# Performance work log

Measured on AMD Instinct MI355X. Metric: run time of the kernel, lower is better.

## Reference

```python
import jax, jax.numpy as jnp
import numpy as np

N = 50000      # total packed nodes
E = 1600000    # edges (no self loops; layers add them)
G = 64         # graphs in the batch
F_IN = 24      # raw node feature dim
D = 64         # hidden dim
H = 4          # attention heads
C = D // H     # 16 channels per head
L = 3          # GAT layers
NEG = 0.2      # LeakyReLU negative slope (GATv2 default)
EPS = 1e-5     # LayerNorm eps


def setup_inputs() -> dict:
    key = jax.random.key(0)
    ks = jax.random.split(key, 16)
    x = jax.random.normal(ks[0], (N, F_IN), jnp.float32)
    src = jax.random.randint(ks[1], (E,), 0, N)
    dst = jax.random.randint(ks[2], (E,), 0, N)
    dst = jnp.where(dst == src, (dst + 1) % N, dst)  # keep edge list self-loop free
    edge_index = jnp.stack([src, dst]).astype(jnp.int32)
    batch = jnp.sort(jax.random.randint(ks[3], (N,), 0, G)).astype(jnp.int32)
    s = 0.1
    return dict(
        x=x, edge_index=edge_index, batch=batch,
        w_in=jax.random.normal(ks[4], (F_IN, D), jnp.float32) * s,
        b_in=jnp.zeros((D,), jnp.float32),
        w_l=jax.random.normal(ks[5], (L, D, D), jnp.float32) * s,
        b_l=jnp.zeros((L, D), jnp.float32),
        w_r=jax.random.normal(ks[6], (L, D, D), jnp.float32) * s,
        b_r=jnp.zeros((L, D), jnp.float32),
        att=jax.random.normal(ks[7], (L, H, C), jnp.float32) * s,
        b_gat=jnp.zeros((L, D), jnp.float32),
        ln_g=jnp.ones((L, D), jnp.float32),
        ln_b=jnp.zeros((L, D), jnp.float32),
        w_g1=jax.random.normal(ks[8], (D, D // 2), jnp.float32) * s,
        b_g1=jnp.zeros((D // 2,), jnp.float32),
        w_g2=jax.random.normal(ks[9], (D // 2, 1), jnp.float32) * s,
        b_g2=jnp.zeros((1,), jnp.float32),
        w_out=jax.random.normal(ks[10], (D, D), jnp.float32) * s,
        b_out=jnp.zeros((D,), jnp.float32),
    )


def _layernorm(h, g, b):
    m = h.mean(-1, keepdims=True)
    v = ((h - m) ** 2).mean(-1, keepdims=True)
    return (h - m) * jax.lax.rsqrt(v + EPS) * g + b


def _gatv2(h, src, dst, wl, bl, wr, br, att, bg):
    n = h.shape[0]
    xl = (h @ wl + bl).reshape(n, H, C)   # source transform
    xr = (h @ wr + br).reshape(n, H, C)   # target transform
    # edge scores: att . leaky_relu(xl[j] + xr[i])  -> [E', H]
    e = jnp.sum(jax.nn.leaky_relu(xl[src] + xr[dst], NEG) * att, axis=-1)
    emax = jax.ops.segment_max(e, dst, num_segments=n)
    ex = jnp.exp(e - emax[dst])
    denom = jax.ops.segment_sum(ex, dst, num_segments=n)
    alpha = ex / denom[dst]               # segment softmax over incoming edges
    out = jax.ops.segment_sum(alpha[:, :, None] * xl[src], dst, num_segments=n)
    return out.reshape(n, D) + bg


def reference(x, edge_index, batch, w_in, b_in, w_l, b_l, w_r, b_r, att, b_gat,
              ln_g, ln_b, w_g1, b_g1, w_g2, b_g2, w_out, b_out):
    n = x.shape[0]
    loops = jnp.arange(n, dtype=edge_index.dtype)
    src = jnp.concatenate([edge_index[0], loops])  # add self loops once
    dst = jnp.concatenate([edge_index[1], loops])
    h = jax.nn.relu(x @ w_in + b_in)
    for i in range(L):
        res = h
        h = _gatv2(h, src, dst, w_l[i], b_l[i], w_r[i], b_r[i], att[i], b_gat[i])
        h = _layernorm(h + res, ln_g[i], ln_b[i])
        if i < L - 1:
            h = jax.nn.relu(h)
    # GlobalAttention pooling: gate MLP -> per-graph softmax -> weighted sum
    gate = jax.nn.relu(h @ w_g1 + b_g1) @ w_g2 + b_g2  # [N, 1]
    gmax = jax.ops.segment_max(gate, batch, num_segments=G)
    ge = jnp.exp(gate - gmax[batch])
    gs = jax.ops.segment_sum(ge, batch, num_segments=G)
    a = ge / jnp.where(gs > 0, gs, 1.0)[batch]
    emb = jax.ops.segment_sum(a * h, batch, num_segments=G)  # [G, D]
    return jax.nn.relu(emb @ w_out + b_out)
```

## Files before the change

kernel.cpp:

```cpp
#include <hip/hip_runtime.h>

#define NEGS   0.2f
#define LN_EPS 1e-5f
#define BSH    7
#define BN     128
#define TILE   4096
#define LOG2E  1.44269504f

typedef const float* __restrict__ fp;
typedef _Float16 v2h __attribute__((ext_vector_type(2)));
typedef _Float16 v8h __attribute__((ext_vector_type(8)));
typedef float    v4f __attribute__((ext_vector_type(4)));

__device__ __forceinline__ v2h u2h(unsigned u){ union{unsigned u; v2h h;} c; c.u = u; return c.h; }
__device__ __forceinline__ unsigned h2u(v2h h){ union{v2h h; unsigned u;} c; c.h = h; return c.u; }

template<int CTRL>
__device__ __forceinline__ float dppadd(float x){
  int y = __builtin_amdgcn_update_dpp(0, __float_as_int(x), CTRL, 0xF, 0xF, true);
  return x + __int_as_float(y);
}
__device__ __forceinline__ float hsum8(float s){
  s = dppadd<0xB1>(s);
  s = dppadd<0x4E>(s);
  s = dppadd<0x141>(s);
  return s;
}
__device__ __forceinline__ float edge_w(v2h v, v2h xrv, v2h att2, float negm8){
  v2h t = v + xrv;
  t = __builtin_elementwise_max(t, t * (_Float16)NEGS);
  float s = hsum8(__builtin_amdgcn_fdot2(t, att2, negm8, false));
  return __builtin_amdgcn_exp2f(s);
}

__global__ __launch_bounds__(256) void k_in(fp x, fp w, fp b, float* __restrict__ h,
                                            unsigned* __restrict__ h16, int N){
  __shared__ float ws[24*64];
  __shared__ float bs[64];
  __shared__ float xs[4][24];
  int tid = threadIdx.x;
  for (int i = tid; i < 24*64; i += 256) ws[i] = w[i];
  if (tid < 64) bs[tid] = b[tid];
  int r = tid >> 6, c = tid & 63;
  int row = blockIdx.x*4 + r;
  if (c < 24 && row < N) xs[r][c] = x[row*24 + c];
  __syncthreads();
  float acc = bs[c];
  #pragma unroll
  for (int k = 0; k < 24; ++k) acc = fmaf(xs[r][k], ws[k*64 + c], acc);
  float y = fmaxf(acc, 0.f);
  float y1 = __shfl_down(y, 1);
  if (row < N){
    h[(size_t)row*64 + c] = y;
    if (!(c & 1)){
      v2h p; p.x = (_Float16)y; p.y = (_Float16)y1;
      h16[(size_t)row*32 + (c >> 1)] = h2u(p);
    }
  }
}

__global__ __launch_bounds__(256) void k_wprep(fp w_l, fp w_r, _Float16* __restrict__ wf){
  int lm = blockIdx.x;
  const float* src = ((lm & 1) ? w_r : w_l) + (lm >> 1)*4096;
  _Float16* dst = wf + lm*4096;
  for (int d = threadIdx.x; d < 4096; d += 256){
    int j = d & 7, l = (d >> 3) & 63, kc = (d >> 9) & 1, nt = d >> 10;
    int k = kc*32 + (l >> 4)*8 + j;
    int n = nt*16 + (l & 15);
    dst[d] = (_Float16)src[k*64 + n];
  }
}

__global__ __launch_bounds__(256) void t_hist(const int* __restrict__ dstA, int* __restrict__ counts,
                                              int E, int K, int ntiles){
  __shared__ int hist[512];
  int t = blockIdx.x, tid = threadIdx.x;
  for (int i = tid; i < K; i += 256) hist[i] = 0;
  __syncthreads();
  int e0 = t*TILE, e1 = min(e0 + TILE, E);
  for (int e = e0 + tid; e < e1; e += 256)
    atomicAdd(&hist[dstA[e] >> BSH], 1);
  __syncthreads();
  for (int i = tid; i < K; i += 256) counts[i*ntiles + t] = hist[i];
}

__global__ __launch_bounds__(512) void s_scan_tiles(int* __restrict__ counts, int* __restrict__ btotal,
                                                    int ntiles){
  __shared__ int s[512];
  int b = blockIdx.x, tid = threadIdx.x;
  int v = (tid < ntiles) ? counts[b*ntiles + tid] : 0;
  s[tid] = v;
  __syncthreads();
  for (int off = 1; off < 512; off <<= 1){
    int t = (tid >= off) ? s[tid - off] : 0;
    __syncthreads();
    s[tid] += t;
    __syncthreads();
  }
  if (tid < ntiles) counts[b*ntiles + tid] = s[tid] - v;
  if (tid == 511) btotal[b] = s[511];
}

__global__ __launch_bounds__(512) void s_scan_buckets(const int* __restrict__ btotal,
                                                      int* __restrict__ bbase, int K, int E){
  __shared__ int s[512];
  int tid = threadIdx.x;
  int v = (tid < K) ? btotal[tid] : 0;
  s[tid] = v;
  __syncthreads();
  for (int off = 1; off < 512; off <<= 1){
    int t = (tid >= off) ? s[tid - off] : 0;
    __syncthreads();
    s[tid] += t;
    __syncthreads();
  }
  if (tid < K) bbase[tid] = s[tid] - v;
  if (tid == 0) bbase[K] = E;
}

__global__ __launch_bounds__(256) void t_scatter(const int* __restrict__ srcA, const int* __restrict__ dstA,
                                                 const int* __restrict__ counts, const int* __restrict__ bbase,
                                                 unsigned* __restrict__ packed, int E, int K, int ntiles){
  __shared__ int gb[512];
  __shared__ int cur[512];
  int t = blockIdx.x, tid = threadIdx.x;
  for (int i = tid; i < K; i += 256){
    gb[i] = bbase[i] + counts[i*ntiles + t];
    cur[i] = 0;
  }
  __syncthreads();
  int e0 = t*TILE, e1 = min(e0 + TILE, E);
  for (int e = e0 + tid; e < e1; e += 256){
    int d = dstA[e], sv = srcA[e];
    int b = d >> BSH;
    int p = atomicAdd(&cur[b], 1);
    packed[gb[b] + p] = ((unsigned)(d & (BN-1)) << 25) | (unsigned)sv;
  }
}

__global__ __launch_bounds__(256) void k_fine(const unsigned* __restrict__ packed, const int* __restrict__ bbase,
                                              int* __restrict__ row_ptr, int* __restrict__ col, int N, int K){
  __shared__ int hist[BN];
  __shared__ int excl[BN];
  int b = blockIdx.x, tid = threadIdx.x;
  int node0 = b << BSH;
  int e_base = bbase[b], e_end = bbase[b+1];
  if (tid < BN) hist[tid] = 0;
  __syncthreads();
  for (int e = e_base + tid; e < e_end; e += 256)
    atomicAdd(&hist[packed[e] >> 25], 1);
  __syncthreads();
  int v = (tid < BN) ? hist[tid] : 0;
  if (tid < BN) excl[tid] = v;
  __syncthreads();
  for (int off = 1; off < BN; off <<= 1){
    int t2 = 0;
    if (tid < BN && tid >= off) t2 = excl[tid - off];
    __syncthreads();
    if (tid < BN) excl[tid] += t2;
    __syncthreads();
  }
  int nn = min(BN, N - node0);
  if (tid < nn) row_ptr[node0 + tid] = e_base + excl[tid] - v;
  if (b == K-1 && tid == 0) row_ptr[N] = e_end;
  if (tid < BN) hist[tid] = excl[tid] - v;
  __syncthreads();
  for (int e = e_base + tid; e < e_end; e += 256){
    unsigned u = packed[e];
    int dl = u >> 25;
    int p = atomicAdd(&hist[dl], 1);
    col[e_base + p] = (int)(u & 0x1FFFFFFu);
  }
}

__global__ __launch_bounds__(256) void k_xfm(const unsigned* __restrict__ h16,
                                             const _Float16* __restrict__ wf,
                                             fp blg, fp brg,
                                             unsigned* __restrict__ xl16, unsigned* __restrict__ xr16, int N){
  int tid = threadIdx.x, wave = tid >> 6, lane = tid & 63;
  int quad = lane >> 4, ln = lane & 15;
  int m0 = blockIdx.x*64 + wave*16;
  if (m0 >= N) return;
  int m = m0 + ln;
  bool mv = m < N;
  v8h a0 = {}, a1 = {};
  if (mv){
    a0 = *(const v8h*)&h16[(size_t)m*32 + quad*4];
    a1 = *(const v8h*)&h16[(size_t)m*32 + 16 + quad*4];
  }
  #pragma unroll
  for (int mat = 0; mat < 2; ++mat){
    const _Float16* wb = wf + mat*4096;
    fp bias = mat ? brg : blg;
    unsigned* dst = mat ? xr16 : xl16;
    #pragma unroll
    for (int nt = 0; nt < 4; ++nt){
      v8h b0 = *(const v8h*)&wb[nt*1024 + lane*8];
      v8h b1 = *(const v8h*)&wb[nt*1024 + 512 + lane*8];
      float bv = bias[nt*16 + ln];
      v4f acc = {bv, bv, bv, bv};
      acc = __builtin_amdgcn_mfma_f32_16x16x32_f16(a0, b0, acc, 0, 0, 0);
      acc = __builtin_amdgcn_mfma_f32_16x16x32_f16(a1, b1, acc, 0, 0, 0);
      #pragma unroll
      for (int r = 0; r < 4; ++r){
        float partner = __shfl_xor(acc[r], 1);
        int node = m0 + quad*4 + r;
        if (!(lane & 1) && node < N){
          v2h p; p.x = (_Float16)acc[r]; p.y = (_Float16)partner;
          dst[(size_t)node*32 + nt*8 + (ln >> 1)] = h2u(p);
        }
      }
    }
  }
}

__global__ __launch_bounds__(256) void k_gat(const unsigned* __restrict__ xl16, const unsigned* __restrict__ xr16,
                                             float* __restrict__ h, unsigned* __restrict__ h16,
                                             const int* __restrict__ row_ptr, const int* __restrict__ col,
                                             fp att, fp bg, fp lng, fp lnb, int N, int do_relu){
  int lane = threadIdx.x & 63;
  int node = blockIdx.x*4 + (threadIdx.x >> 6);
  if (node >= N) return;
  int l = lane & 31;
  bool lower = lane < 32;
  int off = lower ? 0 : 1;
  v2h att2; att2.x = (_Float16)(att[2*l] * LOG2E); att2.y = (_Float16)(att[2*l+1] * LOG2E);
  v2h xrv = u2h(xr16[(size_t)node*32 + l]);
  v2h xlv = u2h(xl16[(size_t)node*32 + l]);
  v2h ts = xlv + xrv;
  ts = __builtin_elementwise_max(ts, ts * (_Float16)NEGS);
  const float m = hsum8(__builtin_amdgcn_fdot2(ts, att2, 0.f, false));
  const float negm8 = m * -0.125f;
  float den0 = lower ? 1.f : 0.f, den1 = 0.f, den2 = 0.f, den3 = 0.f;
  float a0x = lower ? (float)xlv.x : 0.f, a0y = lower ? (float)xlv.y : 0.f;
  float a1x = 0.f, a1y = 0.f, a2x = 0.f, a2y = 0.f, a3x = 0.f, a3y = 0.f;
  int e = row_ptr[node], e1 = row_ptr[node+1];
  for (; e + 16 <= e1; e += 16){
    int j0 = col[e+off],    j1 = col[e+2+off],  j2 = col[e+4+off],  j3 = col[e+6+off];
    int j4 = col[e+8+off],  j5 = col[e+10+off], j6 = col[e+12+off], j7 = col[e+14+off];
    v2h v0 = u2h(xl16[(size_t)j0*32 + l]);
    v2h v1 = u2h(xl16[(size_t)j1*32 + l]);
    v2h v2 = u2h(xl16[(size_t)j2*32 + l]);
    v2h v3 = u2h(xl16[(size_t)j3*32 + l]);
    v2h v4 = u2h(xl16[(size_t)j4*32 + l]);
    v2h v5 = u2h(xl16[(size_t)j5*32 + l]);
    v2h v6 = u2h(xl16[(size_t)j6*32 + l]);
    v2h v7 = u2h(xl16[(size_t)j7*32 + l]);
    float w0 = edge_w(v0, xrv, att2, negm8);
    float w1 = edge_w(v1, xrv, att2, negm8);
    float w2 = edge_w(v2, xrv, att2, negm8);
    float w3 = edge_w(v3, xrv, att2, negm8);
    float w4 = edge_w(v4, xrv, att2, negm8);
    float w5 = edge_w(v5, xrv, att2, negm8);
    float w6 = edge_w(v6, xrv, att2, negm8);
    float w7 = edge_w(v7, xrv, att2, negm8);
    den0 += w0; a0x = fmaf(w0, (float)v0.x, a0x); a0y = fmaf(w0, (float)v0.y, a0y);
    den1 += w1; a1x = fmaf(w1, (float)v1.x, a1x); a1y = fmaf(w1, (float)v1.y, a1y);
    den2 += w2; a2x = fmaf(w2, (float)v2.x, a2x); a2y = fmaf(w2, (float)v2.y, a2y);
    den3 += w3; a3x = fmaf(w3, (float)v3.x, a3x); a3y = fmaf(w3, (float)v3.y, a3y);
    den0 += w4; a0x = fmaf(w4, (float)v4.x, a0x); a0y = fmaf(w4, (float)v4.y, a0y);
    den1 += w5; a1x = fmaf(w5, (float)v5.x, a1x); a1y = fmaf(w5, (float)v5.y, a1y);
    den2 += w6; a2x = fmaf(w6, (float)v6.x, a2x); a2y = fmaf(w6, (float)v6.y, a2y);
    den3 += w7; a3x = fmaf(w7, (float)v7.x, a3x); a3y = fmaf(w7, (float)v7.y, a3y);
  }
  for (; e + 8 <= e1; e += 8){
    int j0 = col[e+off], j1 = col[e+2+off], j2 = col[e+4+off], j3 = col[e+6+off];
    v2h v0 = u2h(xl16[(size_t)j0*32 + l]);
    v2h v1 = u2h(xl16[(size_t)j1*32 + l]);
    v2h v2 = u2h(xl16[(size_t)j2*32 + l]);
    v2h v3 = u2h(xl16[(size_t)j3*32 + l]);
    float w0 = edge_w(v0, xrv, att2, negm8);
    float w1 = edge_w(v1, xrv, att2, negm8);
    float w2 = edge_w(v2, xrv, att2, negm8);
    float w3 = edge_w(v3, xrv, att2, negm8);
    den0 += w0; a0x = fmaf(w0, (float)v0.x, a0x); a0y = fmaf(w0, (float)v0.y, a0y);
    den1 += w1; a1x = fmaf(w1, (float)v1.x, a1x); a1y = fmaf(w1, (float)v1.y, a1y);
    den2 += w2; a2x = fmaf(w2, (float)v2.x, a2x); a2y = fmaf(w2, (float)v2.y, a2y);
    den3 += w3; a3x = fmaf(w3, (float)v3.x, a3x); a3y = fmaf(w3, (float)v3.y, a3y);
  }
  for (; e + 2 <= e1; e += 2){
    int j0 = col[e+off];
    v2h v0 = u2h(xl16[(size_t)j0*32 + l]);
    float w0 = edge_w(v0, xrv, att2, negm8);
    den0 += w0; a0x = fmaf(w0, (float)v0.x, a0x); a0y = fmaf(w0, (float)v0.y, a0y);
  }
  if (e < e1){
    int j0 = col[e];
    v2h v0 = u2h(xl16[(size_t)j0*32 + l]);
    float w0 = edge_w(v0, xrv, att2, negm8);
    if (!lower) w0 = 0.f;
    den0 += w0; a0x = fmaf(w0, (float)v0.x, a0x); a0y = fmaf(w0, (float)v0.y, a0y);
  }
  float den = (den0 + den1) + (den2 + den3);
  float ax = (a0x + a1x) + (a2x + a3x);
  float ay = (a0y + a1y) + (a2y + a3y);
  den += __shfl_xor(den, 32);
  ax  += __shfl_xor(ax, 32);
  ay  += __shfl_xor(ay, 32);
  float inv = 1.f / den;
  float2 bg2 = *(const float2*)&bg[2*l];
  float2 h2  = *(const float2*)&h[(size_t)node*64 + 2*l];
  float ox = ax*inv + bg2.x + h2.x;
  float oy = ay*inv + bg2.y + h2.y;
  float sl = ox + oy;
  #pragma unroll
  for (int o = 1; o < 32; o <<= 1) sl += __shfl_xor(sl, o);
  float mean = sl * (1.f/64.f);
  float dx = ox - mean, dy = oy - mean;
  float vsl = dx*dx + dy*dy;
  #pragma unroll
  for (int o = 1; o < 32; o <<= 1) vsl += __shfl_xor(vsl, o);
  float rs = rsqrtf(vsl * (1.f/64.f) + LN_EPS);
  float2 lg2 = *(const float2*)&lng[2*l];
  float2 lb2 = *(const float2*)&lnb[2*l];
  float yx = dx*rs*lg2.x + lb2.x;
  float yy = dy*rs*lg2.y + lb2.y;
  if (do_relu){ yx = fmaxf(yx, 0.f); yy = fmaxf(yy, 0.f); }
  if (lower){
    float2 y2; y2.x = yx; y2.y = yy;
    *(float2*)&h[(size_t)node*64 + 2*l] = y2;
    v2h p; p.x = (_Float16)yx; p.y = (_Float16)yy;
    h16[(size_t)node*32 + l] = h2u(p);
  }
}

__global__ __launch_bounds__(256) void k_gate(const float* __restrict__ h, fp w1, fp b1, fp w2, fp b2,
                                              float* __restrict__ gate, int N){
  __shared__ float w1s[2048];
  __shared__ float hrow[16][64];
  int tid = threadIdx.x;
  for (int i = tid*4; i < 2048; i += 1024) *(float4*)&w1s[i] = *(const float4*)&w1[i];
  int base = blockIdx.x*16;
  int nrows = min(16, N - base);
  int lim = nrows*64;
  for (int i = tid*4; i < lim; i += 1024)
    *(float4*)&hrow[0][i] = *(const float4*)&h[(size_t)base*64 + i];
  __syncthreads();
  int wave = tid >> 6, lane = tid & 63;
  int j = lane & 31, half = lane >> 5;
  float b1v = b1[j], w2v = w2[j], b2v = b2[0];
  int k0 = half*32;
  #pragma unroll
  for (int it = 0; it < 4; ++it){
    int r = wave*4 + it;
    int node = base + r;
    if (node >= N) break;
    float s = 0.f;
    #pragma unroll 8
    for (int k = k0; k < k0 + 32; ++k) s = fmaf(hrow[r][k], w1s[k*32 + j], s);
    s += __shfl_xor(s, 32);
    float hid = fmaxf(s + b1v, 0.f);
    float contrib = (half == 0) ? hid * w2v : 0.f;
    #pragma unroll
    for (int o = 1; o < 64; o <<= 1) contrib += __shfl_xor(contrib, o);
    if (lane == 0) gate[node] = contrib + b2v;
  }
}

__global__ __launch_bounds__(256) void k_gmax(const float* __restrict__ gate, const int* __restrict__ batch,
                                              float* __restrict__ gmax, float* __restrict__ gsum,
                                              float* __restrict__ embsum, int N){
  int g = blockIdx.x, tid = threadIdx.x;
  if (tid < 64) embsum[g*64 + tid] = 0.f;
  if (tid == 64) gsum[g] = 0.f;
  int lo = 0, hi = N;
  while (lo < hi){ int mid = (lo + hi) >> 1; if (batch[mid] < g) lo = mid + 1; else hi = mid; }
  int start = lo;
  hi = N;
  while (lo < hi){ int mid = (lo + hi) >> 1; if (batch[mid] < g + 1) lo = mid + 1; else hi = mid; }
  int end = lo;
  float m = -3.4e38f;
  for (int i = start + tid; i < end; i += 256) m = fmaxf(m, gate[i]);
  #pragma unroll
  for (int o = 1; o < 64; o <<= 1) m = fmaxf(m, __shfl_xor(m, o));
  __shared__ float ws[4];
  if ((tid & 63) == 0) ws[tid >> 6] = m;
  __syncthreads();
  if (tid == 0) gmax[g] = fmaxf(fmaxf(ws[0], ws[1]), fmaxf(ws[2], ws[3]));
}

__global__ __launch_bounds__(256) void k_emb(const float* __restrict__ h, const float* __restrict__ gate,
                                             const int* __restrict__ batch, const float* __restrict__ gmax,
                                             float* __restrict__ gsum, float* __restrict__ embsum, int N){
  int lane = threadIdx.x & 63;
  int wv = blockIdx.x*4 + (threadIdx.x >> 6);
  int s = wv*64;
  if (s >= N) return;
  int e = min(s + 64, N);
  int cur = batch[s];
  float gm = gmax[cur];
  float acc = 0.f, asum = 0.f;
  for (int i = s; i < e; ++i){
    int g = batch[i];
    if (g != cur){
      atomicAdd(&embsum[cur*64 + lane], acc);
      if (lane == 0) atomicAdd(&gsum[cur], asum);
      acc = 0.f; asum = 0.f; cur = g; gm = gmax[g];
    }
    float a = __expf(gate[i] - gm);
    acc = fmaf(a, h[(size_t)i*64 + lane], acc);
    asum += a;
  }
  atomicAdd(&embsum[cur*64 + lane], acc);
  if (lane == 0) atomicAdd(&gsum[cur], asum);
}

__global__ __launch_bounds__(64) void k_out(const float* __restrict__ embsum, const float* __restrict__ gsum,
                                            fp w_out, fp b_out, float* __restrict__ out, int G){
  int g = blockIdx.x, lane = threadIdx.x;
  __shared__ float emb[64];
  float gs = gsum[g];
  float inv = (gs > 0.f) ? 1.f/gs : 1.f;
  emb[lane] = embsum[g*64 + lane] * inv;
  __syncthreads();
  float o2 = b_out[lane];
  #pragma unroll 8
  for (int d = 0; d < 64; ++d) o2 = fmaf(emb[d], w_out[d*64 + lane], o2);
  out[g*64 + lane] = fmaxf(o2, 0.f);
}

extern "C" void kernel_launch(void* const* d_in, const int* in_sizes, int n_in,
                              void* d_out, int out_size, void* d_ws, size_t ws_size,
                              hipStream_t stream) {
  const int N = in_sizes[0] / 24;
  const int E = in_sizes[1] / 2;
  const int G = out_size / 64;
  const int K = (N + BN - 1) >> BSH;
  const int ntiles = (E + TILE - 1) / TILE;

  fp x      = (fp)d_in[0];
  const int* edge  = (const int*)d_in[1];
  const int* batch = (const int*)d_in[2];
  fp w_in   = (fp)d_in[3];
  fp b_in   = (fp)d_in[4];
  fp w_l    = (fp)d_in[5];
  fp b_l    = (fp)d_in[6];
  fp w_r    = (fp)d_in[7];
  fp b_r    = (fp)d_in[8];
  fp att    = (fp)d_in[9];
  fp b_gat  = (fp)d_in[10];
  fp ln_g   = (fp)d_in[11];
  fp ln_b   = (fp)d_in[12];
  fp w_g1   = (fp)d_in[13];
  fp b_g1   = (fp)d_in[14];
  fp w_g2   = (fp)d_in[15];
  fp b_g2   = (fp)d_in[16];
  fp w_out  = (fp)d_in[17];
  fp b_out  = (fp)d_in[18];
  float* out = (float*)d_out;

  char* wp = (char*)d_ws;
  auto alloc = [&](size_t bytes) -> char* {
    char* p = wp; wp += (bytes + 255) & ~(size_t)255; return p;
  };
  float*    h       = (float*)    alloc((size_t)N*64*sizeof(float));
  unsigned* h16     = (unsigned*) alloc((size_t)N*32*sizeof(unsigned));
  unsigned* xl16    = (unsigned*) alloc((size_t)N*32*sizeof(unsigned));
  unsigned* xr16    = (unsigned*) alloc((size_t)N*32*sizeof(unsigned));
  int*      col     = (int*)      alloc((size_t)E*sizeof(int));
  unsigned* packed  = (unsigned*) alloc((size_t)E*sizeof(unsigned));
  int*      counts  = (int*)      alloc((size_t)K*ntiles*sizeof(int));
  int*      btotal  = (int*)      alloc((size_t)K*sizeof(int));
  int*      bbase   = (int*)      alloc((size_t)(K+1)*sizeof(int));
  int*      row_ptr = (int*)      alloc((size_t)(N+1)*sizeof(int));
  float*    gate    = (float*)    alloc((size_t)N*sizeof(float));
  float*    gmax    = (float*)    alloc((size_t)G*sizeof(float));
  float*    gsum    = (float*)    alloc((size_t)(G + G*64)*sizeof(float));
  float*    embsum  = gsum + G;
  _Float16* wf      = (_Float16*) alloc((size_t)3*2*4096*sizeof(_Float16));

  const int* srcA = edge;
  const int* dstA = edge + E;

  k_in<<<(N + 3)/4, 256, 0, stream>>>(x, w_in, b_in, h, h16, N);
  k_wprep<<<6, 256, 0, stream>>>(w_l, w_r, wf);

  t_hist<<<ntiles, 256, 0, stream>>>(dstA, counts, E, K, ntiles);
  s_scan_tiles<<<K, 512, 0, stream>>>(counts, btotal, ntiles);
  s_scan_buckets<<<1, 512, 0, stream>>>(btotal, bbase, K, E);
  t_scatter<<<ntiles, 256, 0, stream>>>(srcA, dstA, counts, bbase, packed, E, K, ntiles);
  k_fine<<<K, 256, 0, stream>>>(packed, bbase, row_ptr, col, N, K);

  for (int i = 0; i < 3; ++i){
    k_xfm<<<(N + 63)/64, 256, 0, stream>>>(h16, wf + i*8192, b_l + i*64, b_r + i*64,
                                           xl16, xr16, N);
    k_gat<<<(N + 3)/4, 256, 0, stream>>>(xl16, xr16, h, h16, row_ptr, col,
                                         att + i*64, b_gat + i*64, ln_g + i*64, ln_b + i*64,
                                         N, i < 2 ? 1 : 0);
  }
  k_gate<<<(N + 15)/16, 256, 0, stream>>>(h, w_g1, b_g1, w_g2, b_g2, gate, N);
  k_gmax<<<G, 256, 0, stream>>>(gate, batch, gmax, gsum, embsum, N);
  k_emb<<<(N + 255)/256, 256, 0, stream>>>(h, gate, batch, gmax, gsum, embsum, N);
  k_out<<<G, 64, 0, stream>>>(embsum, gsum, w_out, b_out, out, G);
}
```

Baseline: 384.3 us.

## Remap GAT wave to 8 edges x 8 lanes with 16-byte gathers

The per-node GAT aggregation moves from two half-waves, each reading 4-byte chunks per lane, to eight lane groups of eight lanes. Each lane gathers 16 bytes (eight fp16 channels) of a neighbour row and computes the head score with four fdot2 plus one DPP add, in place of three DPP steps. This uses wider gather loads, fewer cross-lane ops per edge and more edges in flight, at the cost of more accumulator registers and a larger final cross-group shuffle reduction. The attention vector is pre-scaled and converted to fp16 once in the weight-prep kernel rather than in every thread.

```diff
diff --git a/kernel.cpp b/kernel.cpp
--- a/kernel.cpp
+++ b/kernel.cpp
@@ -20,16 +20,24 @@
   int y = __builtin_amdgcn_update_dpp(0, __float_as_int(x), CTRL, 0xF, 0xF, true);
   return x + __int_as_float(y);
 }
-__device__ __forceinline__ float hsum8(float s){
-  s = dppadd<0xB1>(s);
-  s = dppadd<0x4E>(s);
-  s = dppadd<0x141>(s);
+
+__device__ __forceinline__ float dot8(v8h a, v8h b, float init){
+  union U { v8h v; v2h h[4]; };
+  U ua; ua.v = a;
+  U ub; ub.v = b;
+  float s = init;
+  #pragma unroll
+  for (int i = 0; i < 4; ++i) s = __builtin_amdgcn_fdot2(ua.h[i], ub.h[i], s, false);
   return s;
 }
-__device__ __forceinline__ float edge_w(v2h v, v2h xrv, v2h att2, float negm8){
-  v2h t = v + xrv;
-  t = __builtin_elementwise_max(t, t * (_Float16)NEGS);
-  float s = hsum8(__builtin_amdgcn_fdot2(t, att2, negm8, false));
+
+__device__ __forceinline__ v8h leaky8(v8h t){
+  return __builtin_elementwise_max(t, t * (_Float16)NEGS);
+}
+
+__device__ __forceinline__ float edge_w8(v8h v, v8h xr8, v8h att8, float negm2){
+  v8h t = leaky8(v + xr8);
+  float s = dppadd<0xB1>(dot8(t, att8, negm2));
   return __builtin_amdgcn_exp2f(s);
 }
 
@@ -59,8 +67,13 @@
   }
 }
 
-__global__ __launch_bounds__(256) void k_wprep(fp w_l, fp w_r, _Float16* __restrict__ wf){
+__global__ __launch_bounds__(256) void k_wprep(fp w_l, fp w_r, fp att, _Float16* __restrict__ wf,
+                                               _Float16* __restrict__ att16){
   int lm = blockIdx.x;
+  if (lm < 3){
+    for (int d = threadIdx.x; d < 64; d += 256)
+      att16[lm*64 + d] = (_Float16)(att[lm*64 + d] * LOG2E);
+  }
   const float* src = ((lm & 1) ? w_r : w_l) + (lm >> 1)*4096;
   _Float16* dst = wf + lm*4096;
   for (int d = threadIdx.x; d < 4096; d += 256){
@@ -217,110 +230,100 @@
 __global__ __launch_bounds__(256) void k_gat(const unsigned* __restrict__ xl16, const unsigned* __restrict__ xr16,
                                              float* __restrict__ h, unsigned* __restrict__ h16,
                                              const int* __restrict__ row_ptr, const int* __restrict__ col,
-                                             fp att, fp bg, fp lng, fp lnb, int N, int do_relu){
+                                             const _Float16* __restrict__ att16, fp bg, fp lng, fp lnb,
+                                             int N, int do_relu){
   int lane = threadIdx.x & 63;
   int node = blockIdx.x*4 + (threadIdx.x >> 6);
   if (node >= N) return;
-  int l = lane & 31;
-  bool lower = lane < 32;
-  int off = lower ? 0 : 1;
-  v2h att2; att2.x = (_Float16)(att[2*l] * LOG2E); att2.y = (_Float16)(att[2*l+1] * LOG2E);
-  v2h xrv = u2h(xr16[(size_t)node*32 + l]);
-  v2h xlv = u2h(xl16[(size_t)node*32 + l]);
-  v2h ts = xlv + xrv;
-  ts = __builtin_elementwise_max(ts, ts * (_Float16)NEGS);
-  const float m = hsum8(__builtin_amdgcn_fdot2(ts, att2, 0.f, false));
-  const float negm8 = m * -0.125f;
-  float den0 = lower ? 1.f : 0.f, den1 = 0.f, den2 = 0.f, den3 = 0.f;
-  float a0x = lower ? (float)xlv.x : 0.f, a0y = lower ? (float)xlv.y : 0.f;
-  float a1x = 0.f, a1y = 0.f, a2x = 0.f, a2y = 0.f, a3x = 0.f, a3y = 0.f;
+  int g = lane >> 3;
+  int s = lane & 7;
+
+  v8h att8 = *(const v8h*)&att16[s*8];
+  v8h xr8  = *(const v8h*)&xr16[(size_t)node*32 + s*4];
+  v8h xl8  = *(const v8h*)&xl16[(size_t)node*32 + s*4];
+
+  float m = dppadd<0xB1>(dot8(leaky8(xl8 + xr8), att8, 0.f));
+  float negm2 = m * -0.5f;
+
+  float den = (g == 0) ? 1.f : 0.f;
+  float acc[8];
+  #pragma unroll
+  for (int i = 0; i < 8; ++i) acc[i] = (g == 0) ? (float)xl8[i] : 0.f;
+
   int e = row_ptr[node], e1 = row_ptr[node+1];
   for (; e + 16 <= e1; e += 16){
-    int j0 = col[e+off],    j1 = col[e+2+off],  j2 = col[e+4+off],  j3 = col[e+6+off];
-    int j4 = col[e+8+off],  j5 = col[e+10+off], j6 = col[e+12+off], j7 = col[e+14+off];
-    v2h v0 = u2h(xl16[(size_t)j0*32 + l]);
-    v2h v1 = u2h(xl16[(size_t)j1*32 + l]);
-    v2h v2 = u2h(xl16[(size_t)j2*32 + l]);
-    v2h v3 = u2h(xl16[(size_t)j3*32 + l]);
-    v2h v4 = u2h(xl16[(size_t)j4*32 + l]);
-    v2h v5 = u2h(xl16[(size_t)j5*32 + l]);
-    v2h v6 = u2h(xl16[(size_t)j6*32 + l]);
-    v2h v7 = u2h(xl16[(size_t)j7*32 + l]);
-    float w0 = edge_w(v0, xrv, att2, negm8);
-    float w1 = edge_w(v1, xrv, att2, negm8);
-    float w2 = edge_w(v2, xrv, att2, negm8);
-    float w3 = edge_w(v3, xrv, att2, negm8);
-    float w4 = edge_w(v4, xrv, att2, negm8);
-    float w5 = edge_w(v5, xrv, att2, negm8);
-    float w6 = edge_w(v6, xrv, att2, negm8);
-    float w7 = edge_w(v7, xrv, att2, negm8);
-    den0 += w0; a0x = fmaf(w0, (float)v0.x, a0x); a0y = fmaf(w0, (float)v0.y, a0y);
-    den1 += w1; a1x = fmaf(w1, (float)v1.x, a1x); a1y = fmaf(w1, (float)v1.y, a1y);
-    den2 += w2; a2x = fmaf(w2, (float)v2.x, a2x); a2y = fmaf(w2, (float)v2.y, a2y);
-    den3 += w3; a3x = fmaf(w3, (float)v3.x, a3x); a3y = fmaf(w3, (float)v3.y, a3y);
-    den0 += w4; a0x = fmaf(w4, (float)v4.x, a0x); a0y = fmaf(w4, (float)v4.y, a0y);
-    den1 += w5; a1x = fmaf(w5, (float)v5.x, a1x); a1y = fmaf(w5, (float)v5.y, a1y);
-    den2 += w6; a2x = fmaf(w6, (float)v6.x, a2x); a2y = fmaf(w6, (float)v6.y, a2y);
-    den3 += w7; a3x = fmaf(w7, (float)v7.x, a3x); a3y = fmaf(w7, (float)v7.y, a3y);
-  }
-  for (; e + 8 <= e1; e += 8){
-    int j0 = col[e+off], j1 = col[e+2+off], j2 = col[e+4+off], j3 = col[e+6+off];
-    v2h v0 = u2h(xl16[(size_t)j0*32 + l]);
-    v2h v1 = u2h(xl16[(size_t)j1*32 + l]);
-    v2h v2 = u2h(xl16[(size_t)j2*32 + l]);
-    v2h v3 = u2h(xl16[(size_t)j3*32 + l]);
-    float w0 = edge_w(v0, xrv, att2, negm8);
-    float w1 = edge_w(v1, xrv, att2, negm8);
-    float w2 = edge_w(v2, xrv, att2, negm8);
-    float w3 = edge_w(v3, xrv, att2, negm8);
-    den0 += w0; a0x = fmaf(w0, (float)v0.x, a0x); a0y = fmaf(w0, (float)v0.y, a0y);
-    den1 += w1; a1x = fmaf(w1, (float)v1.x, a1x); a1y = fmaf(w1, (float)v1.y, a1y);
-    den2 += w2; a2x = fmaf(w2, (float)v2.x, a2x); a2y = fmaf(w2, (float)v2.y, a2y);
-    den3 += w3; a3x = fmaf(w3, (float)v3.x, a3x); a3y = fmaf(w3, (float)v3.y, a3y);
-  }
-  for (; e + 2 <= e1; e += 2){
-    int j0 = col[e+off];
-    v2h v0 = u2h(xl16[(size_t)j0*32 + l]);
-    float w0 = edge_w(v0, xrv, att2, negm8);
-    den0 += w0; a0x = fmaf(w0, (float)v0.x, a0x); a0y = fmaf(w0, (float)v0.y, a0y);
-  }
-  if (e < e1){
-    int j0 = col[e];
-    v2h v0 = u2h(xl16[(size_t)j0*32 + l]);
-    float w0 = edge_w(v0, xrv, att2, negm8);
-    if (!lower) w0 = 0.f;
-    den0 += w0; a0x = fmaf(w0, (float)v0.x, a0x); a0y = fmaf(w0, (float)v0.y, a0y);
-  }
-  float den = (den0 + den1) + (den2 + den3);
-  float ax = (a0x + a1x) + (a2x + a3x);
-  float ay = (a0y + a1y) + (a2y + a3y);
-  den += __shfl_xor(den, 32);
-  ax  += __shfl_xor(ax, 32);
-  ay  += __shfl_xor(ay, 32);
+    int j0 = col[e + g];
+    int j1 = col[e + 8 + g];
+    v8h v0 = *(const v8h*)&xl16[(size_t)j0*32 + s*4];
+    v8h v1 = *(const v8h*)&xl16[(size_t)j1*32 + s*4];
+    float w0 = edge_w8(v0, xr8, att8, negm2);
+    float w1 = edge_w8(v1, xr8, att8, negm2);
+    den += w0; den += w1;
+    #pragma unroll
+    for (int i = 0; i < 8; ++i){
+      acc[i] = fmaf(w0, (float)v0[i], acc[i]);
+      acc[i] = fmaf(w1, (float)v1[i], acc[i]);
+    }
+  }
+  for (; e < e1; e += 8){
+    int idx = e + g;
+    bool valid = idx < e1;
+    int j0 = col[valid ? idx : e];
+    v8h v0 = *(const v8h*)&xl16[(size_t)j0*32 + s*4];
+    float w0 = edge_w8(v0, xr8, att8, negm2);
+    w0 = valid ? w0 : 0.f;
+    den += w0;
+    #pragma unroll
+    for (int i = 0; i < 8; ++i) acc[i] = fmaf(w0, (float)v0[i], acc[i]);
+  }
+
+  #pragma unroll
+  for (int o = 8; o < 64; o <<= 1){
+    den += __shfl_xor(den, o);
+    #pragma unroll
+    for (int i = 0; i < 8; ++i) acc[i] += __shfl_xor(acc[i], o);
+  }
   float inv = 1.f / den;
-  float2 bg2 = *(const float2*)&bg[2*l];
-  float2 h2  = *(const float2*)&h[(size_t)node*64 + 2*l];
-  float ox = ax*inv + bg2.x + h2.x;
-  float oy = ay*inv + bg2.y + h2.y;
-  float sl = ox + oy;
-  #pragma unroll
-  for (int o = 1; o < 32; o <<= 1) sl += __shfl_xor(sl, o);
+
+  float4 bgA = *(const float4*)&bg[s*8];
+  float4 bgB = *(const float4*)&bg[s*8 + 4];
+  float4 hA  = *(const float4*)&h[(size_t)node*64 + s*8];
+  float4 hB  = *(const float4*)&h[(size_t)node*64 + s*8 + 4];
+  float res8[8] = {hA.x + bgA.x, hA.y + bgA.y, hA.z + bgA.z, hA.w + bgA.w,
+                   hB.x + bgB.x, hB.y + bgB.y, hB.z + bgB.z, hB.w + bgB.w};
+  float o8[8];
+  float sl = 0.f;
+  #pragma unroll
+  for (int i = 0; i < 8; ++i){ o8[i] = fmaf(acc[i], inv, res8[i]); sl += o8[i]; }
+  #pragma unroll
+  for (int o = 1; o < 8; o <<= 1) sl += __shfl_xor(sl, o);
   float mean = sl * (1.f/64.f);
-  float dx = ox - mean, dy = oy - mean;
-  float vsl = dx*dx + dy*dy;
-  #pragma unroll
-  for (int o = 1; o < 32; o <<= 1) vsl += __shfl_xor(vsl, o);
+  float vsl = 0.f;
+  #pragma unroll
+  for (int i = 0; i < 8; ++i){ o8[i] -= mean; vsl = fmaf(o8[i], o8[i], vsl); }
+  #pragma unroll
+  for (int o = 1; o < 8; o <<= 1) vsl += __shfl_xor(vsl, o);
   float rs = rsqrtf(vsl * (1.f/64.f) + LN_EPS);
-  float2 lg2 = *(const float2*)&lng[2*l];
-  float2 lb2 = *(const float2*)&lnb[2*l];
-  float yx = dx*rs*lg2.x + lb2.x;
-  float yy = dy*rs*lg2.y + lb2.y;
-  if (do_relu){ yx = fmaxf(yx, 0.f); yy = fmaxf(yy, 0.f); }
-  if (lower){
-    float2 y2; y2.x = yx; y2.y = yy;
-    *(float2*)&h[(size_t)node*64 + 2*l] = y2;
-    v2h p; p.x = (_Float16)yx; p.y = (_Float16)yy;
-    h16[(size_t)node*32 + l] = h2u(p);
+
+  if (g == 0){
+    float4 lgA = *(const float4*)&lng[s*8], lgB = *(const float4*)&lng[s*8 + 4];
+    float4 lbA = *(const float4*)&lnb[s*8], lbB = *(const float4*)&lnb[s*8 + 4];
+    float lg8[8] = {lgA.x, lgA.y, lgA.z, lgA.w, lgB.x, lgB.y, lgB.z, lgB.w};
+    float lb8[8] = {lbA.x, lbA.y, lbA.z, lbA.w, lbB.x, lbB.y, lbB.z, lbB.w};
+    float y[8];
+    #pragma unroll
+    for (int i = 0; i < 8; ++i){
+      y[i] = fmaf(o8[i]*rs, lg8[i], lb8[i]);
+      if (do_relu) y[i] = fmaxf(y[i], 0.f);
+    }
+    float4 yA = {y[0], y[1], y[2], y[3]};
+    float4 yB = {y[4], y[5], y[6], y[7]};
+    *(float4*)&h[(size_t)node*64 + s*8]     = yA;
+    *(float4*)&h[(size_t)node*64 + s*8 + 4] = yB;
+    v8h p;
+    #pragma unroll
+    for (int i = 0; i < 8; ++i) p[i] = (_Float16)y[i];
+    *(v8h*)&h16[(size_t)node*32 + s*4] = p;
   }
 }
 
@@ -468,12 +471,13 @@
   float*    gsum    = (float*)    alloc((size_t)(G + G*64)*sizeof(float));
   float*    embsum  = gsum + G;
   _Float16* wf      = (_Float16*) alloc((size_t)3*2*4096*sizeof(_Float16));
+  _Float16* att16g  = (_Float16*) alloc((size_t)3*64*sizeof(_Float16));
 
   const int* srcA = edge;
   const int* dstA = edge + E;
 
   k_in<<<(N + 3)/4, 256, 0, stream>>>(x, w_in, b_in, h, h16, N);
-  k_wprep<<<6, 256, 0, stream>>>(w_l, w_r, wf);
+  k_wprep<<<6, 256, 0, stream>>>(w_l, w_r, att, wf, att16g);
 
   t_hist<<<ntiles, 256, 0, stream>>>(dstA, counts, E, K, ntiles);
   s_scan_tiles<<<K, 512, 0, stream>>>(counts, btotal, ntiles);
@@ -485,7 +489,7 @@
     k_xfm<<<(N + 63)/64, 256, 0, stream>>>(h16, wf + i*8192, b_l + i*64, b_r + i*64,
                                            xl16, xr16, N);
     k_gat<<<(N + 3)/4, 256, 0, stream>>>(xl16, xr16, h, h16, row_ptr, col,
-                                         att + i*64, b_gat + i*64, ln_g + i*64, ln_b + i*64,
+                                         att16g + i*64, b_gat + i*64, ln_g + i*64, ln_b + i*64,
                                          N, i < 2 ? 1 : 0);
   }
   k_gate<<<(N + 15)/16, 256, 0, stream>>>(h, w_g1, b_g1, w_g2, b_g2, gate, N);
```

After: 360.8 us. 6.1% less time.
